# Performance work log

Measured on AMD Instinct MI355X. Metric: run time of the kernel, lower is better.

## Reference

```python
import jax, jax.numpy as jnp
import numpy as np

B, S, E = 4, 2048, 1024

def setup_inputs() -> dict:
    key = jax.random.key(0)
    ks = jax.random.split(key, 4)
    scale = 1.0 / np.sqrt(E)
    x = jax.random.normal(ks[0], (B, S, E), dtype=jnp.float32)
    Wq = jax.random.normal(ks[1], (E, E), dtype=jnp.float32) * scale
    Wk = jax.random.normal(ks[2], (E, E), dtype=jnp.float32) * scale
    Wv = jax.random.normal(ks[3], (E, E), dtype=jnp.float32) * scale
    bq = jnp.zeros((E,), dtype=jnp.float32)
    bk = jnp.zeros((E,), dtype=jnp.float32)
    bv = jnp.zeros((E,), dtype=jnp.float32)
    # causal mask: 1 where attention allowed, 0 where blocked (masked_fill(mask==0, -inf))
    mask = jnp.tril(jnp.ones((S, S), dtype=jnp.int32))
    return {"x": x, "mask": mask, "Wq": Wq, "bq": bq, "Wk": Wk, "bk": bk, "Wv": Wv, "bv": bv}

def reference(x, mask, Wq, bq, Wk, bk, Wv, bv):
    # x: (B, S, E); mask: (S, S) int, 0 -> -inf. Matches torch nn.Linear: x @ W.T + b
    Q = jnp.einsum('bse,fe->bsf', x, Wq) + bq
    K = jnp.einsum('bse,fe->bsf', x, Wk) + bk
    V = jnp.einsum('bse,fe->bsf', x, Wv) + bv
    inv_sqrt_e = 1.0 / jnp.sqrt(jnp.asarray(x.shape[-1], dtype=x.dtype))
    scores = jnp.einsum('bqe,bke->bqk', Q, K) * inv_sqrt_e  # (B, S, S)
    scores = jnp.where(mask[None, :, :] == 0, jnp.asarray(-jnp.inf, scores.dtype), scores)
    attn = jax.nn.softmax(scores, axis=-1)
    out = jnp.einsum('bqk,bke->bqe', attn, V)  # (B, S, E)
    return out
```

## Files before the change

### kernel.cpp

```cpp
#include <hip/hip_runtime.h>

#define B_ 4
#define S_ 2048
#define E_ 1024

typedef __attribute__((ext_vector_type(8))) short short8;
typedef __attribute__((ext_vector_type(4))) float f32x4;

__device__ __forceinline__ unsigned short f2bu(float f) {
  unsigned u = __builtin_bit_cast(unsigned, f);
  u = (u + 0x7FFFu + ((u >> 16) & 1u)) >> 16;
  return (unsigned short)u;
}

__device__ __forceinline__ void gload_lds16(const void* g, void* l) {
  __builtin_amdgcn_global_load_lds(
      (const __attribute__((address_space(1))) void*)g,
      (__attribute__((address_space(3))) void*)l, 16, 0, 0);
}

__global__ __launch_bounds__(256) void cvt_f32_bf16(
    const float* __restrict__ in, unsigned short* __restrict__ out, int n) {
  int i = blockIdx.x * 256 + threadIdx.x;
  if (i * 4 >= n) return;
  float4 v = ((const float4*)in)[i];
  ushort4 o;
  o.x = f2bu(v.x); o.y = f2bu(v.y); o.z = f2bu(v.z); o.w = f2bu(v.w);
  ((ushort4*)out)[i] = o;
}

__global__ __launch_bounds__(256) void cvt_w3(
    const float* __restrict__ w0, const float* __restrict__ w1,
    const float* __restrict__ w2, unsigned short* __restrict__ out, int n) {
  int z = blockIdx.z;
  const float* in = (z == 0) ? w0 : (z == 1) ? w1 : w2;
  int i = blockIdx.x * 256 + threadIdx.x;
  if (i * 4 >= n) return;
  float4 v = ((const float4*)in)[i];
  ushort4 o;
  o.x = f2bu(v.x); o.y = f2bu(v.y); o.z = f2bu(v.z); o.w = f2bu(v.w);
  ((ushort4*)(out + (long)z * n))[i] = o;
}

template<int MODE>
__global__ __launch_bounds__(256, 3) void gemm_bt(
    const unsigned short* __restrict__ A, long sAz, int lda,
    const unsigned short* __restrict__ B, long sBz, int ldb,
    const float* __restrict__ bias0, const float* __restrict__ bias1,
    const float* __restrict__ bias2,
    void* __restrict__ C0, void* __restrict__ C1, void* __restrict__ C2,
    long sCz, int ldc, int K, float scale) {
  constexpr int BM = 128, BN = 128, BK = 64;
  __shared__ unsigned short lA[BM * BK];
  __shared__ unsigned short lB[BN * BK];
  int bm, bn;
  int bz = blockIdx.z;
  if constexpr (MODE == 1) {
    int t = blockIdx.x;
    bm = (int)((sqrtf(8.f * t + 1.f) - 1.f) * 0.5f);
    while ((bm + 1) * (bm + 2) / 2 <= t) bm++;
    while (bm * (bm + 1) / 2 > t) bm--;
    bn = t - bm * (bm + 1) / 2;
  } else {
    bm = blockIdx.y; bn = blockIdx.x;
  }
  const unsigned short* Ab = A + (long)bz * sAz + (long)bm * BM * lda;
  const unsigned short* Bb = B + (long)bz * sBz + (long)bn * BN * ldb;
  int Keff = (MODE == 2) ? min(K, (bm + 1) * BM) : K;

  int tid = threadIdx.x;
  int l = tid & 63, w = tid >> 6;
  int wm = w >> 1, wn = w & 1;

  int srow = l >> 3;
  int schunk = (l & 7) * 8;
  const unsigned short* ga[4];
  const unsigned short* gb[4];
  unsigned short* lad[4];
  unsigned short* lbd[4];
#pragma unroll
  for (int i = 0; i < 4; i++) {
    int seg = i * 4 + w;
    int row = seg * 8 + srow;
    ga[i] = Ab + (long)row * lda + schunk;
    gb[i] = Bb + (long)row * ldb + schunk;
    lad[i] = &lA[seg * 512];
    lbd[i] = &lB[seg * 512];
  }
  int aoff[4], boff[4];
#pragma unroll
  for (int i = 0; i < 4; i++) {
    aoff[i] = (wm * 64 + i * 16 + (l & 15)) * BK + (l >> 4) * 8;
    boff[i] = (wn * 64 + i * 16 + (l & 15)) * BK + (l >> 4) * 8;
  }

  f32x4 acc[4][4] = {};
  f32x4 accd[4] = {};
  short8 ones;
#pragma unroll
  for (int z = 0; z < 8; z++) ones[z] = (short)0x3F80;

  for (int k0 = 0; k0 < Keff; k0 += BK) {
    __syncthreads();
#pragma unroll
    for (int i = 0; i < 4; i++) {
      gload_lds16(ga[i], lad[i]);
      gload_lds16(gb[i], lbd[i]);
    }
#pragma unroll
    for (int i = 0; i < 4; i++) { ga[i] += BK; gb[i] += BK; }
    __syncthreads();
#pragma unroll
    for (int kk = 0; kk < 2; kk++) {
      short8 af[4], bf[4];
#pragma unroll
      for (int i = 0; i < 4; i++) af[i] = *(const short8*)&lA[aoff[i] + kk * 32];
#pragma unroll
      for (int j = 0; j < 4; j++) bf[j] = *(const short8*)&lB[boff[j] + kk * 32];
#pragma unroll
      for (int i = 0; i < 4; i++)
#pragma unroll
        for (int j = 0; j < 4; j++)
          acc[i][j] = __builtin_amdgcn_mfma_f32_16x16x32_bf16(af[i], bf[j], acc[i][j], 0, 0, 0);
      if constexpr (MODE == 2) {
#pragma unroll
        for (int i = 0; i < 4; i++)
          accd[i] = __builtin_amdgcn_mfma_f32_16x16x32_bf16(af[i], ones, accd[i], 0, 0, 0);
      }
    }
  }

  int rh = l >> 4, cl = l & 15;
  long rowbase = (long)bm * BM + wm * 64 + rh * 4;
  int colbase = bn * BN + wn * 64 + cl;

  if constexpr (MODE == 0) {
    int seg = bn >> 3;
    const float* bias = (seg == 0) ? bias0 : (seg == 1) ? bias1 : bias2;
#pragma unroll
    for (int j = 0; j < 4; j++) {
      int c = colbase + j * 16;
      int cl_ = c & 1023;
      float bv_ = bias[cl_];
#pragma unroll
      for (int i = 0; i < 4; i++) {
        long r0 = rowbase + i * 16;
        f32x4 v = acc[i][j];
        if (seg < 2) {
          unsigned short* Ch = (unsigned short*)((seg == 0) ? C0 : C1);
#pragma unroll
          for (int t = 0; t < 4; t++)
            Ch[(r0 + t) * (long)E_ + cl_] = f2bu(v[t] + bv_);
        } else {
          unsigned short* Vt = (unsigned short*)C2;
          ushort4 pk;
          pk.x = f2bu(v[0] + bv_);
          pk.y = f2bu(v[1] + bv_);
          pk.z = f2bu(v[2] + bv_);
          pk.w = f2bu(v[3] + bv_);
          *(ushort4*)(Vt + (long)cl_ * (B_ * S_) + r0) = pk;
        }
      }
    }
  } else if constexpr (MODE == 1) {
    unsigned short* Ph = (unsigned short*)C0 + (long)bz * sCz;
#pragma unroll
    for (int j = 0; j < 4; j++) {
      int c = colbase + j * 16;
#pragma unroll
      for (int i = 0; i < 4; i++) {
        int r0 = (int)rowbase + i * 16;
        f32x4 v = acc[i][j];
#pragma unroll
        for (int t = 0; t < 4; t++) {
          int r = r0 + t;
          float p = (c <= r) ? __expf(v[t] * scale) : 0.f;
          Ph[(long)r * ldc + c] = f2bu(p);
        }
      }
    }
  } else {
    float* Cf = (float*)C0 + (long)bz * sCz;
#pragma unroll
    for (int j = 0; j < 4; j++) {
      int c = colbase + j * 16;
#pragma unroll
      for (int i = 0; i < 4; i++) {
        long r0 = rowbase + i * 16;
        f32x4 v = acc[i][j];
        f32x4 d = accd[i];
#pragma unroll
        for (int t = 0; t < 4; t++)
          Cf[(r0 + t) * (long)ldc + c] = v[t] / d[t];
      }
    }
  }
}

extern "C" void kernel_launch(void* const* d_in, const int* in_sizes, int n_in,
                              void* d_out, int out_size, void* d_ws, size_t ws_size,
                              hipStream_t stream) {
  const float* x  = (const float*)d_in[0];
  const float* Wq = (const float*)d_in[2];
  const float* bq = (const float*)d_in[3];
  const float* Wk = (const float*)d_in[4];
  const float* bk = (const float*)d_in[5];
  const float* Wv = (const float*)d_in[6];
  const float* bv = (const float*)d_in[7];
  float* out = (float*)d_out;

  const long NX = (long)B_ * S_ * E_;
  const long NW = (long)E_ * E_;
  unsigned short* xb  = (unsigned short*)d_ws;
  unsigned short* wqb = xb + NX;
  unsigned short* Qb  = wqb + 3 * NW;
  unsigned short* Kb  = Qb + NX;
  unsigned short* Vtb = Kb + NX;
  unsigned short* Pb  = Vtb + NX;

  cvt_f32_bf16<<<8192, 256, 0, stream>>>(x, xb, (int)NX);
  cvt_w3<<<dim3(1024, 1, 3), 256, 0, stream>>>(Wq, Wk, Wv, wqb, (int)NW);

  gemm_bt<0><<<dim3(24, 64, 1), 256, 0, stream>>>(
      xb, 0, E_, wqb, 0, E_, bq, bk, bv,
      Qb, Kb, Vtb, 0, E_, E_, 1.f);

  gemm_bt<1><<<dim3(136, 1, 4), 256, 0, stream>>>(
      Qb, (long)S_ * E_, E_, Kb, (long)S_ * E_, E_, nullptr, nullptr, nullptr,
      Pb, nullptr, nullptr, (long)S_ * S_, S_, E_, 0.03125f);

  gemm_bt<2><<<dim3(8, 16, 4), 256, 0, stream>>>(
      Pb, (long)S_ * S_, S_,
      Vtb, (long)S_, B_ * S_, nullptr, nullptr, nullptr,
      out, nullptr, nullptr, (long)S_ * E_, E_, S_, 1.f);
}
```

Baseline: 175.0 us.

## Replace QKV projection GEMM with 256x128 tile, 8-wave double-buffered pipelined kernel

Adds a dedicated QKV projection kernel that uses 256x128 output tiles with 8 waves per 512-thread block. It double-buffers the global-to-LDS loads across 96KB of dynamic shared memory with XOR-swizzled columns to avoid bank conflicts. The K loop is split into phases with explicit barriers, waitcnt and setprio so that staging the next tiles overlaps the MFMA work. The goal is to cut the single-buffered load-then-compute stalls of the generic GEMM on the projection step, which is the largest matmul. In exchange there is more LDS use per block, fewer blocks in the grid (768), and fragile hand scheduling.

```diff
diff --git a/kernel.cpp b/kernel.cpp
--- a/kernel.cpp
+++ b/kernel.cpp
@@ -42,14 +42,135 @@
   ((ushort4*)(out + (long)z * n))[i] = o;
 }
 
+__global__ __launch_bounds__(512, 2) void qkv8(
+    const unsigned short* __restrict__ A, const unsigned short* __restrict__ W,
+    const float* __restrict__ bq, const float* __restrict__ bk,
+    const float* __restrict__ bv,
+    unsigned short* __restrict__ Qo, unsigned short* __restrict__ Ko,
+    unsigned short* __restrict__ Vt) {
+  extern __shared__ char smem[];
+  constexpr int NT = 16;
+  int tid = threadIdx.x;
+  int l = tid & 63, w = tid >> 6;
+  int wm = w >> 2, wn = w & 3;
+  int tm = blockIdx.y, tn = blockIdx.x;
+
+  int scol = 8 * ((l & 7) ^ ((l >> 3) & 7));
+  const unsigned short* Ag = A + (long)tm * 256 * 1024 + scol;
+  const unsigned short* Bg = W + (long)tn * 128 * 1024 + scol;
+
+#define STG_A(tt, h, q)                                                     \
+  gload_lds16(Ag + ((long)(h) * 128 + (w * 2 + (q)) * 8 + (l >> 3)) * 1024  \
+                  + (long)(tt) * 64,                                        \
+              smem + ((tt) & 1) * 32768 + (h) * 16384 + (w * 2 + (q)) * 1024)
+#define STG_B(tt, q)                                                        \
+  gload_lds16(Bg + ((long)(w * 2 + (q)) * 8 + (l >> 3)) * 1024              \
+                  + (long)(tt) * 64,                                        \
+              smem + 65536 + ((tt) & 1) * 16384 + (w * 2 + (q)) * 1024)
+
+  int xorc = (l & 7) << 4;
+  int c0 = ((l >> 4) * 16) ^ xorc;
+  int c1 = (64 + (l >> 4) * 16) ^ xorc;
+  int arowbase = (wm * 128 + (l & 15)) * 128;
+  int browbase = (wn * 32 + (l & 15)) * 128;
+
+  f32x4 acc[8][2] = {};
+  short8 a[4][2], b[2][2];
+
+  STG_A(0, 0, 0); STG_A(0, 0, 1); STG_A(0, 1, 0); STG_A(0, 1, 1);
+  STG_B(0, 0);    STG_B(0, 1);
+  STG_A(1, 0, 0); STG_A(1, 0, 1); STG_A(1, 1, 0); STG_A(1, 1, 1);
+
+#define PHASE_TAIL(h, j)                                                    \
+  asm volatile("" ::: "memory");                                            \
+  __builtin_amdgcn_s_barrier();                                             \
+  asm volatile("s_waitcnt lgkmcnt(0)" ::: "memory");                        \
+  __builtin_amdgcn_sched_barrier(0);                                        \
+  __builtin_amdgcn_s_setprio(1);                                            \
+  _Pragma("unroll")                                                         \
+  for (int ii = 0; ii < 4; ii++) {                                          \
+    acc[(h) * 4 + ii][j] = __builtin_amdgcn_mfma_f32_16x16x32_bf16(         \
+        a[ii][0], b[j][0], acc[(h) * 4 + ii][j], 0, 0, 0);                  \
+    acc[(h) * 4 + ii][j] = __builtin_amdgcn_mfma_f32_16x16x32_bf16(         \
+        a[ii][1], b[j][1], acc[(h) * 4 + ii][j], 0, 0, 0);                  \
+  }                                                                         \
+  __builtin_amdgcn_s_setprio(0);                                            \
+  __builtin_amdgcn_sched_barrier(0);                                        \
+  asm volatile("" ::: "memory");                                            \
+  __builtin_amdgcn_s_barrier();
+
+  for (int t = 0; t < NT; ++t) {
+    const char* Ad = smem + (t & 1) * 32768;
+    const char* Bd = smem + 65536 + (t & 1) * 16384;
+    if (t < NT - 1) asm volatile("s_waitcnt vmcnt(4)" ::: "memory");
+    else            asm volatile("s_waitcnt vmcnt(0)" ::: "memory");
+    __builtin_amdgcn_s_barrier();
+
+#pragma unroll
+    for (int ii = 0; ii < 4; ii++) {
+      a[ii][0] = *(const short8*)(Ad + arowbase + ii * 2048 + c0);
+      a[ii][1] = *(const short8*)(Ad + arowbase + ii * 2048 + c1);
+    }
+    b[0][0] = *(const short8*)(Bd + browbase + c0);
+    b[0][1] = *(const short8*)(Bd + browbase + c1);
+    if (t + 1 < NT) { STG_B(t + 1, 0); STG_B(t + 1, 1); }
+    PHASE_TAIL(0, 0)
+
+    b[1][0] = *(const short8*)(Bd + browbase + 2048 + c0);
+    b[1][1] = *(const short8*)(Bd + browbase + 2048 + c1);
+    PHASE_TAIL(0, 1)
+
+#pragma unroll
+    for (int ii = 0; ii < 4; ii++) {
+      a[ii][0] = *(const short8*)(Ad + arowbase + 8192 + ii * 2048 + c0);
+      a[ii][1] = *(const short8*)(Ad + arowbase + 8192 + ii * 2048 + c1);
+    }
+    PHASE_TAIL(1, 0)
+
+    if (t + 2 < NT) { STG_A(t + 2, 0, 0); STG_A(t + 2, 0, 1);
+                      STG_A(t + 2, 1, 0); STG_A(t + 2, 1, 1); }
+    PHASE_TAIL(1, 1)
+  }
+
+  int rh = l >> 4, cl = l & 15;
+  int colbase = tn * 128 + wn * 32 + cl;
+  long rowbase = (long)tm * 256 + wm * 128 + rh * 4;
+  int seg = tn >> 3;
+  const float* bias = (seg == 0) ? bq : (seg == 1) ? bk : bv;
+#pragma unroll
+  for (int j = 0; j < 2; j++) {
+    int c = colbase + j * 16;
+    int cm = c & 1023;
+    float bv_ = bias[cm];
+#pragma unroll
+    for (int i = 0; i < 8; i++) {
+      long r0 = rowbase + i * 16;
+      f32x4 v = acc[i][j];
+      if (seg < 2) {
+        unsigned short* Ch = seg ? Ko : Qo;
+#pragma unroll
+        for (int t4 = 0; t4 < 4; t4++)
+          Ch[(r0 + t4) * (long)E_ + cm] = f2bu(v[t4] + bv_);
+      } else {
+        ushort4 pk;
+        pk.x = f2bu(v[0] + bv_);
+        pk.y = f2bu(v[1] + bv_);
+        pk.z = f2bu(v[2] + bv_);
+        pk.w = f2bu(v[3] + bv_);
+        *(ushort4*)(Vt + (long)cm * (B_ * S_) + r0) = pk;
+      }
+    }
+  }
+#undef STG_A
+#undef STG_B
+#undef PHASE_TAIL
+}
+
 template<int MODE>
 __global__ __launch_bounds__(256, 3) void gemm_bt(
     const unsigned short* __restrict__ A, long sAz, int lda,
     const unsigned short* __restrict__ B, long sBz, int ldb,
-    const float* __restrict__ bias0, const float* __restrict__ bias1,
-    const float* __restrict__ bias2,
-    void* __restrict__ C0, void* __restrict__ C1, void* __restrict__ C2,
-    long sCz, int ldc, int K, float scale) {
+    void* __restrict__ C0, long sCz, int ldc, int K, float scale) {
   constexpr int BM = 128, BN = 128, BK = 64;
   __shared__ unsigned short lA[BM * BK];
   __shared__ unsigned short lB[BN * BK];
@@ -134,35 +255,7 @@
   long rowbase = (long)bm * BM + wm * 64 + rh * 4;
   int colbase = bn * BN + wn * 64 + cl;
 
-  if constexpr (MODE == 0) {
-    int seg = bn >> 3;
-    const float* bias = (seg == 0) ? bias0 : (seg == 1) ? bias1 : bias2;
-#pragma unroll
-    for (int j = 0; j < 4; j++) {
-      int c = colbase + j * 16;
-      int cl_ = c & 1023;
-      float bv_ = bias[cl_];
-#pragma unroll
-      for (int i = 0; i < 4; i++) {
-        long r0 = rowbase + i * 16;
-        f32x4 v = acc[i][j];
-        if (seg < 2) {
-          unsigned short* Ch = (unsigned short*)((seg == 0) ? C0 : C1);
-#pragma unroll
-          for (int t = 0; t < 4; t++)
-            Ch[(r0 + t) * (long)E_ + cl_] = f2bu(v[t] + bv_);
-        } else {
-          unsigned short* Vt = (unsigned short*)C2;
-          ushort4 pk;
-          pk.x = f2bu(v[0] + bv_);
-          pk.y = f2bu(v[1] + bv_);
-          pk.z = f2bu(v[2] + bv_);
-          pk.w = f2bu(v[3] + bv_);
-          *(ushort4*)(Vt + (long)cl_ * (B_ * S_) + r0) = pk;
-        }
-      }
-    }
-  } else if constexpr (MODE == 1) {
+  if constexpr (MODE == 1) {
     unsigned short* Ph = (unsigned short*)C0 + (long)bz * sCz;
 #pragma unroll
     for (int j = 0; j < 4; j++) {
@@ -218,19 +311,25 @@
   unsigned short* Vtb = Kb + NX;
   unsigned short* Pb  = Vtb + NX;
 
+  static int smem_set = 0;
+  if (!smem_set) {
+    hipFuncSetAttribute((const void*)qkv8,
+                        hipFuncAttributeMaxDynamicSharedMemorySize, 98304);
+    smem_set = 1;
+  }
+
   cvt_f32_bf16<<<8192, 256, 0, stream>>>(x, xb, (int)NX);
   cvt_w3<<<dim3(1024, 1, 3), 256, 0, stream>>>(Wq, Wk, Wv, wqb, (int)NW);
 
-  gemm_bt<0><<<dim3(24, 64, 1), 256, 0, stream>>>(
-      xb, 0, E_, wqb, 0, E_, bq, bk, bv,
-      Qb, Kb, Vtb, 0, E_, E_, 1.f);
+  qkv8<<<dim3(24, 32), 512, 98304, stream>>>(
+      xb, wqb, bq, bk, bv, Qb, Kb, Vtb);
 
   gemm_bt<1><<<dim3(136, 1, 4), 256, 0, stream>>>(
-      Qb, (long)S_ * E_, E_, Kb, (long)S_ * E_, E_, nullptr, nullptr, nullptr,
-      Pb, nullptr, nullptr, (long)S_ * S_, S_, E_, 0.03125f);
+      Qb, (long)S_ * E_, E_, Kb, (long)S_ * E_, E_,
+      Pb, (long)S_ * S_, S_, E_, 0.03125f);
 
   gemm_bt<2><<<dim3(8, 16, 4), 256, 0, stream>>>(
       Pb, (long)S_ * S_, S_,
-      Vtb, (long)S_, B_ * S_, nullptr, nullptr, nullptr,
-      out, nullptr, nullptr, (long)S_ * E_, E_, S_, 1.f);
-}
+      Vtb, (long)S_, B_ * S_,
+      out, (long)S_ * E_, E_, S_, 1.f);
+}
```

Result: no change. 176.8 us (+1.0%).
